# Kernel tuning notes

Measured on AMD Instinct MI355X. Metric: run time of the kernel, lower is better.

Reference implementation:

```python
import jax, jax.numpy as jnp
import numpy as np

N_NODES = 100000
N_EDGES = 1600000
D_IN = 128
D_HID = 128
D_OUT = 128
ORIG = 90000


def setup_inputs() -> dict:
    key = jax.random.key(0)
    ks = jax.random.split(key, 8)
    x = jax.random.normal(ks[0], (N_NODES, D_IN), dtype=jnp.float32)
    edge_index = jax.random.randint(ks[1], (2, N_EDGES), 0, N_NODES, dtype=jnp.int64)
    # Glorot-ish scaled weights; PyG SAGEConv: lin_l (with bias) on aggregated, lin_r (no bias) on root
    s1 = 1.0 / np.sqrt(D_IN)
    s2 = 1.0 / np.sqrt(D_HID)
    Wl1 = jax.random.normal(ks[2], (D_IN, D_HID), dtype=jnp.float32) * s1
    bl1 = jnp.zeros((D_HID,), dtype=jnp.float32)
    Wr1 = jax.random.normal(ks[3], (D_IN, D_HID), dtype=jnp.float32) * s1
    Wl2 = jax.random.normal(ks[4], (D_HID, D_OUT), dtype=jnp.float32) * s2
    bl2 = jnp.zeros((D_OUT,), dtype=jnp.float32)
    Wr2 = jax.random.normal(ks[5], (D_HID, D_OUT), dtype=jnp.float32) * s2
    return {"x": x, "edge_index": edge_index, "original_size": ORIG,
            "Wl1": Wl1, "bl1": bl1, "Wr1": Wr1,
            "Wl2": Wl2, "bl2": bl2, "Wr2": Wr2}


def _sage_conv(x, src, dst, Wl, bl, Wr):
    # PyG SAGEConv (aggr='mean'): out = lin_l(mean_{j in N(i)} x_j) + lin_r(x_i)
    n = x.shape[0]
    msgs = x[src]                                            # [E, d] gather
    ssum = jax.ops.segment_sum(msgs, dst, num_segments=n)    # [N, d]
    cnt = jax.ops.segment_sum(jnp.ones((src.shape[0],), dtype=x.dtype), dst,
                              num_segments=n)                # [N]
    mean = ssum / jnp.maximum(cnt, 1.0)[:, None]             # 0 for isolated nodes
    return mean @ Wl + bl + x @ Wr


def reference(x, edge_index, original_size, Wl1, bl1, Wr1, Wl2, bl2, Wr2):
    src, dst = edge_index[0], edge_index[1]
    h = _sage_conv(x, src, dst, Wl1, bl1, Wr1)
    h = _sage_conv(h, src, dst, Wl2, bl2, Wr2)
    return h[:original_size]
```

## Files before the change

### kernel.cpp

```cpp
#include <hip/hip_runtime.h>

#define NN 100000
#define DD 128

typedef __attribute__((ext_vector_type(8))) short bf16x8;
typedef __attribute__((ext_vector_type(4))) float f32x4;
typedef __attribute__((ext_vector_type(2))) float f32x2;

__device__ __forceinline__ float bf2f(unsigned short u) {
    union { unsigned int i; float f; } v;
    v.i = ((unsigned int)u) << 16;
    return v.f;
}

__device__ __forceinline__ unsigned short f2bf(float f) {
    union { float f; unsigned int i; } v;
    v.f = f;
    unsigned int x = v.i;
    return (unsigned short)((x + 0x7FFFu + ((x >> 16) & 1u)) >> 16);
}

__device__ __forceinline__ float2 load2(const float* p, int i2) {
    return ((const float2*)p)[i2];
}

__device__ __forceinline__ f32x2 cvt2(unsigned int u) {
    union { unsigned int i; float f; } lo, hi;
    lo.i = u << 16;
    hi.i = u & 0xffff0000u;
    return (f32x2){lo.f, hi.f};
}

__device__ __forceinline__ bf16x8 load8_bf(const unsigned short* p) {
    return *((const bf16x8*)p);
}
__device__ __forceinline__ bf16x8 load8_bf(const float* p) {
    float4 a = ((const float4*)p)[0];
    float4 b = ((const float4*)p)[1];
    bf16x8 r;
    r[0] = (short)f2bf(a.x); r[1] = (short)f2bf(a.y);
    r[2] = (short)f2bf(a.z); r[3] = (short)f2bf(a.w);
    r[4] = (short)f2bf(b.x); r[5] = (short)f2bf(b.y);
    r[6] = (short)f2bf(b.z); r[7] = (short)f2bf(b.w);
    return r;
}


#define PCH 16
#define NBUKMAX 512
#define CAP 12288

__global__ __launch_bounds__(256) void hist_buckets(
    const int* __restrict__ ei, int E, int* __restrict__ bcnt, int nbuk) {
    __shared__ int is64_s;
    __shared__ int hl[NBUKMAX];
    int tid = threadIdx.x;
    for (int i = tid; i < nbuk; i += 256) hl[i] = 0;
    if (tid < 64) {
        int ok = (ei[2 * tid + 1] == 0);
        int all = __all(ok);
        if (tid == 0) is64_s = all;
    }
    __syncthreads();
    int is64 = is64_s;
    int e0 = blockIdx.x * (256 * PCH) + tid;
#pragma unroll
    for (int c = 0; c < PCH; c++) {
        int e = e0 + c * 256;
        if (e < E) {
            int d = is64 ? ei[2 * (E + e)] : ei[E + e];
            atomicAdd(&hl[d >> 8], 1);
        }
    }
    __syncthreads();
    for (int i = tid; i < nbuk; i += 256) {
        int v = hl[i];
        if (v) atomicAdd(&bcnt[i], v);
    }
}

__global__ void scan_buckets(const int* __restrict__ bcnt, int nbuk,
                             int* __restrict__ boff, int* __restrict__ offN, int E) {
    __shared__ int wsum[8];
    int tid = threadIdx.x;
    int lane = tid & 63, wid = tid >> 6;
    int v = (tid < nbuk) ? bcnt[tid] : 0;
    int s = v;
#pragma unroll
    for (int dl = 1; dl < 64; dl <<= 1) {
        int t = __shfl_up(s, dl, 64);
        if (lane >= dl) s += t;
    }
    if (lane == 63) wsum[wid] = s;
    __syncthreads();
    int w = 0;
#pragma unroll
    for (int i = 0; i < 8; i++) w += (i < wid) ? wsum[i] : 0;
    if (tid < nbuk) boff[tid] = w + s - v;
    if (tid == nbuk - 1) boff[nbuk] = w + s;
    if (tid == 0) offN[0] = E;
}

__global__ __launch_bounds__(256) void partition_edges(
    const int* __restrict__ ei, int E, const int* __restrict__ boff,
    int* __restrict__ bcur, unsigned long long* __restrict__ pairs, int nbuk) {
    __shared__ int is64_s;
    __shared__ int cntb[NBUKMAX];
    __shared__ int baseb[NBUKMAX];
    __shared__ int boffb[NBUKMAX];
    int tid = threadIdx.x;
    for (int i = tid; i < nbuk; i += 256) {
        cntb[i] = 0;
        boffb[i] = boff[i];
    }
    if (tid < 64) {
        int ok = (ei[2 * tid + 1] == 0);
        int all = __all(ok);
        if (tid == 0) is64_s = all;
    }
    __syncthreads();
    int is64 = is64_s;
    int e0 = blockIdx.x * (256 * PCH) + tid;

    int dv[PCH], sv[PCH], bl[PCH];
    bool va[PCH];
#pragma unroll
    for (int c = 0; c < PCH; c++) {
        int e = e0 + c * 256;
        va[c] = (e < E);
        dv[c] = va[c] ? (is64 ? ei[2 * (E + e)] : ei[E + e]) : 0;
        sv[c] = va[c] ? (is64 ? ei[2 * e] : ei[e]) : 0;
        bl[c] = 0;
    }
#pragma unroll
    for (int c = 0; c < PCH; c++) {
        if (va[c]) {
            int b = dv[c] >> 8;
            int l = atomicAdd(&cntb[b], 1);
            bl[c] = (b << 16) | l;
        }
    }
    __syncthreads();
    for (int i = tid; i < nbuk; i += 256) {
        int cb = cntb[i];
        baseb[i] = cb ? atomicAdd(&bcur[i], cb) : 0;
    }
    __syncthreads();
#pragma unroll
    for (int c = 0; c < PCH; c++) {
        if (va[c]) {
            int b = bl[c] >> 16, l = bl[c] & 0xffff;
            pairs[(size_t)(boffb[b] + baseb[b] + l)] =
                ((unsigned long long)(unsigned int)dv[c] << 32) | (unsigned int)sv[c];
        }
    }
}

__global__ __launch_bounds__(256) void build_csr(
    const unsigned long long* __restrict__ pairs, const int* __restrict__ boff,
    int* __restrict__ off, int* __restrict__ csr, int* __restrict__ cur, int N) {
    int b = blockIdx.x;
    int lo = b << 8;
    if (lo >= N) return;
    int hi = min(lo + 256, N);
    int nn = hi - lo;
    int base = boff[b];
    int pcount = boff[b + 1] - base;

    __shared__ int cnt_l[256];
    __shared__ int start_l[256];
    __shared__ int cur_l[256];
    __shared__ int wsum[4];
    __shared__ int lds_csr[CAP];

    int tid = threadIdx.x;
    cnt_l[tid] = 0;
    __syncthreads();

    for (int i = tid; i < pcount; i += 256) {
        int d = (int)(pairs[base + i] >> 32);
        atomicAdd(&cnt_l[d - lo], 1);
    }
    __syncthreads();

    int v = cnt_l[tid];
    int s = v;
    int lane = tid & 63, wid = tid >> 6;
#pragma unroll
    for (int dl = 1; dl < 64; dl <<= 1) {
        int t = __shfl_up(s, dl, 64);
        if (lane >= dl) s += t;
    }
    if (lane == 63) wsum[wid] = s;
    __syncthreads();
    int w = 0;
#pragma unroll
    for (int i = 0; i < 4; i++) w += (i < wid) ? wsum[i] : 0;
    int excl = w + s - v;
    start_l[tid] = excl;
    cur_l[tid] = excl;
    if (tid < nn) off[lo + tid] = base + excl;
    __syncthreads();

    if (pcount <= CAP) {
        for (int i = tid; i < pcount; i += 256) {
            unsigned long long p = pairs[base + i];
            int d = (int)(p >> 32) - lo;
            int pos = atomicAdd(&cur_l[d], 1);
            lds_csr[pos] = (int)(p & 0xffffffffu);
        }
        __syncthreads();
        for (int i = tid; i < pcount; i += 256) csr[base + i] = lds_csr[i];
    } else {
        for (int i = tid; i < pcount; i += 256) {
            unsigned long long p = pairs[base + i];
            int dg = (int)(p >> 32);
            int q = atomicAdd(&cur[dg], 1);
            csr[base + start_l[dg - lo] + q] = (int)(p & 0xffffffffu);
        }
    }
}

__global__ void cast_bf16(const float* __restrict__ in, unsigned short* __restrict__ out,
                          int n4) {
    int i = blockIdx.x * blockDim.x + threadIdx.x;
    if (i >= n4) return;
    float4 v = ((const float4*)in)[i];
    ushort4 o;
    o.x = f2bf(v.x); o.y = f2bf(v.y); o.z = f2bf(v.z); o.w = f2bf(v.w);
    ((ushort4*)out)[i] = o;
}

__global__ void prep_weights(const float* __restrict__ Wl1, const float* __restrict__ Wr1,
                             const float* __restrict__ Wl2, const float* __restrict__ Wr2,
                             unsigned short* __restrict__ Wt1, unsigned short* __restrict__ Wt2) {
    __shared__ float t[32][33];
    int which = blockIdx.x >> 4;
    const float* W = (which == 0) ? Wl1 : (which == 1) ? Wr1 : (which == 2) ? Wl2 : Wr2;
    unsigned short* Wt = (which < 2) ? Wt1 : Wt2;
    int koff = (which & 1) * 128;
    int b = blockIdx.x & 15;
    int bx = b & 3, by = b >> 2;
    int c = threadIdx.x & 31, r8 = threadIdx.x >> 5;
#pragma unroll
    for (int i = 0; i < 4; i++) {
        int r = r8 + i * 8;
        t[r][c] = W[(by * 32 + r) * 128 + bx * 32 + c];
    }
    __syncthreads();
#pragma unroll
    for (int i = 0; i < 4; i++) {
        int r = r8 + i * 8;
        int fi = bx * 32 + r;
        int kk = koff + by * 32 + c;
        int idx = ((fi >> 4) * 8 + (kk >> 5)) * 512 + ((kk >> 3) & 3) * 128
                + (fi & 15) * 8 + (kk & 7);
        Wt[idx] = f2bf(t[c][r]);
    }
}

#define ACC8(u) do { \
    acc[0] += cvt2((u).x); acc[1] += cvt2((u).y); \
    acc[2] += cvt2((u).z); acc[3] += cvt2((u).w); } while (0)

__global__ __launch_bounds__(256) void aggregate_bf(
    const unsigned short* __restrict__ feat,
    const int* __restrict__ off, const int* __restrict__ csr,
    unsigned short* __restrict__ mean, int N, const int* __restrict__ limp) {
    int lim = limp ? min(N, limp[0]) : N;
    int node = blockIdx.x * 4 + (threadIdx.x >> 6);
    if (node >= lim) return;
    int lane = threadIdx.x & 63;
    int e = lane >> 4, q = lane & 15;
    int s0 = off[node], s1 = off[node + 1];
    unsigned qoff = (unsigned)q << 4;
    const char* fb = (const char*)feat;

    f32x2 acc[4];
#pragma unroll
    for (int t = 0; t < 4; t++) acc[t] = (f32x2){0.f, 0.f};

    for (int c0 = s0; c0 < s1; c0 += 64) {
        int cdeg = min(64, s1 - c0);
        int cr = (lane < cdeg) ? csr[c0 + lane] : 0;
        int nfull = cdeg >> 4, rem = cdeg & 15;
        for (int b = 0; b < nfull; b++) {
            int i0 = b * 16 + e;
            unsigned o0 = ((unsigned)__shfl(cr, i0, 64) << 8) + qoff;
            unsigned o1 = ((unsigned)__shfl(cr, i0 + 4, 64) << 8) + qoff;
            unsigned o2 = ((unsigned)__shfl(cr, i0 + 8, 64) << 8) + qoff;
            unsigned o3 = ((unsigned)__shfl(cr, i0 + 12, 64) << 8) + qoff;
            uint4 C0 = *(const uint4*)(fb + o0);
            uint4 C1 = *(const uint4*)(fb + o1);
            uint4 C2 = *(const uint4*)(fb + o2);
            uint4 C3 = *(const uint4*)(fb + o3);
            ACC8(C0); ACC8(C1); ACC8(C2); ACC8(C3);
        }
        if (rem) {
            int i0 = nfull * 16 + e;
            int t0 = __shfl(cr, i0, 64), t1 = __shfl(cr, i0 + 4, 64),
                t2 = __shfl(cr, i0 + 8, 64), t3 = __shfl(cr, i0 + 12, 64);
            uint4 C0 = make_uint4(0, 0, 0, 0), C1 = C0, C2 = C0, C3 = C0;
            if (i0 < cdeg)      C0 = *(const uint4*)(fb + ((((unsigned)t0) << 8) + qoff));
            if (i0 + 4 < cdeg)  C1 = *(const uint4*)(fb + ((((unsigned)t1) << 8) + qoff));
            if (i0 + 8 < cdeg)  C2 = *(const uint4*)(fb + ((((unsigned)t2) << 8) + qoff));
            if (i0 + 12 < cdeg) C3 = *(const uint4*)(fb + ((((unsigned)t3) << 8) + qoff));
            ACC8(C0); ACC8(C1); ACC8(C2); ACC8(C3);
        }
    }

#pragma unroll
    for (int t = 0; t < 4; t++) {
        union { f32x2 v; double d; } a, b;
        a.v = acc[t];
        b.d = __shfl_xor(a.d, 16, 64); a.v += b.v;
        b.d = __shfl_xor(a.d, 32, 64); a.v += b.v;
        acc[t] = a.v;
    }

    int deg = s1 - s0;
    float inv = (deg > 0) ? (1.0f / (float)deg) : 0.0f;
    if (e == 0) {
        f32x2 iv = (f32x2){inv, inv};
        f32x2 m0 = acc[0] * iv, m1 = acc[1] * iv,
              m2 = acc[2] * iv, m3 = acc[3] * iv;
        uint4 w;
        asm("v_cvt_pk_bf16_f32 %0, %1, %2" : "=v"(w.x) : "v"(m0.x), "v"(m0.y));
        asm("v_cvt_pk_bf16_f32 %0, %1, %2" : "=v"(w.y) : "v"(m1.x), "v"(m1.y));
        asm("v_cvt_pk_bf16_f32 %0, %1, %2" : "=v"(w.z) : "v"(m2.x), "v"(m2.y));
        asm("v_cvt_pk_bf16_f32 %0, %1, %2" : "=v"(w.w) : "v"(m3.x), "v"(m3.y));
        *((uint4*)((char*)mean + (size_t)node * 256 + qoff)) = w;
    }
}

__global__ void aggregate_f32(const float* __restrict__ feat,
                              const int* __restrict__ off, const int* __restrict__ csr,
                              unsigned short* __restrict__ mean, int N) {
    int node = blockIdx.x * (blockDim.x >> 6) + (threadIdx.x >> 6);
    if (node >= N) return;
    int lane = threadIdx.x & 63;
    int s0 = off[node], s1 = off[node + 1];
    float ax = 0.f, ay = 0.f;
    for (int j = s0; j < s1; j++) {
        int s = csr[j];
        float2 v = load2(feat, s * 64 + lane);
        ax += v.x; ay += v.y;
    }
    float inv = (s1 > s0) ? (1.0f / (float)(s1 - s0)) : 0.0f;
    unsigned int p = (unsigned int)f2bf(ax * inv) | ((unsigned int)f2bf(ay * inv) << 16);
    ((unsigned int*)mean)[node * 64 + lane] = p;
}

template <typename TA2, typename TO>
__global__ __launch_bounds__(256) void gemm_mfma(
    const unsigned short* __restrict__ A1, const TA2* __restrict__ A2,
    const unsigned short* __restrict__ Wt, const float* __restrict__ bias,
    TO* __restrict__ out, int Arows, int Nlimit, const int* __restrict__ origp) {
    int lim = Nlimit;
    if (origp) lim = min(lim, origp[0]);
    int n0 = blockIdx.x * 64;
    if (n0 >= lim) return;

    int tid = threadIdx.x;
    int lane = tid & 63;
    int wid = tid >> 6;
    int wm = wid >> 1, wn = wid & 1;
    int qd = lane >> 4, l16 = lane & 15;

    int r0 = min(n0 + wm * 32 + l16, Arows - 1);
    int r1 = min(n0 + wm * 32 + 16 + l16, Arows - 1);

    f32x4 acc[2][4];
#pragma unroll
    for (int a = 0; a < 2; a++)
#pragma unroll
        for (int b = 0; b < 4; b++) acc[a][b] = (f32x4){0.f, 0.f, 0.f, 0.f};

#pragma unroll
    for (int ks = 0; ks < 8; ks++) {
        int kb = (ks & 3) * 32;
        bf16x8 a0, a1;
        if (ks < 4) {
            a0 = load8_bf(A1 + (size_t)r0 * 128 + kb + qd * 8);
            a1 = load8_bf(A1 + (size_t)r1 * 128 + kb + qd * 8);
        } else {
            a0 = load8_bf(A2 + (size_t)r0 * 128 + kb + qd * 8);
            a1 = load8_bf(A2 + (size_t)r1 * 128 + kb + qd * 8);
        }
#pragma unroll
        for (int tn = 0; tn < 4; tn++) {
            int slot = (wn * 4 + tn) * 8 + ks;
            bf16x8 bfrag = *((const bf16x8*)(Wt + slot * 512 + lane * 8));
            acc[0][tn] = __builtin_amdgcn_mfma_f32_16x16x32_bf16(a0, bfrag, acc[0][tn], 0, 0, 0);
            acc[1][tn] = __builtin_amdgcn_mfma_f32_16x16x32_bf16(a1, bfrag, acc[1][tn], 0, 0, 0);
        }
    }

#pragma unroll
    for (int tn = 0; tn < 4; tn++) {
        int f = wn * 64 + tn * 16 + l16;
        float bv = bias[f];
#pragma unroll
        for (int tm = 0; tm < 2; tm++) {
#pragma unroll
            for (int r = 0; r < 4; r++) {
                int n = n0 + wm * 32 + tm * 16 + qd * 4 + r;
                if (n < lim) {
                    float val = acc[tm][tn][r] + bv;
                    if constexpr (__is_same(TO, float))
                        out[n * 128 + f] = val;
                    else
                        out[n * 128 + f] = f2bf(val);
                }
            }
        }
    }
}

extern "C" void kernel_launch(void* const* d_in, const int* in_sizes, int n_in,
                              void* d_out, int out_size, void* d_ws, size_t ws_size,
                              hipStream_t stream) {
    const float* x   = (const float*)d_in[0];
    const int*   ei  = (const int*)d_in[1];
    const int*   org = (const int*)d_in[2];
    const float* Wl1 = (const float*)d_in[3];
    const float* bl1 = (const float*)d_in[4];
    const float* Wr1 = (const float*)d_in[5];
    const float* Wl2 = (const float*)d_in[6];
    const float* bl2 = (const float*)d_in[7];
    const float* Wr2 = (const float*)d_in[8];
    float* out = (float*)d_out;

    const int N = in_sizes[0] / DD;
    const int E = in_sizes[1] / 2;

    size_t szFeat = (size_t)N * DD * 2;
    size_t szBase = 2 * szFeat
                  + 2 * 65536
                  + (size_t)N * 4 + 4096
                  + (size_t)(N + 1) * 4
                  + 4096
                  + (size_t)E * 4;
    bool big = ws_size >= szBase + szFeat + 4096;

    char* ws = (char*)d_ws;
    unsigned short* mean = (unsigned short*)ws;  ws += szFeat;
    unsigned short* h    = (unsigned short*)ws;  ws += szFeat;
    unsigned short* xb   = nullptr;
    if (big) { xb = (unsigned short*)ws; ws += szFeat; }
    unsigned short* Wt1 = (unsigned short*)ws;  ws += 65536;
    unsigned short* Wt2 = (unsigned short*)ws;  ws += 65536;
    int* cur  = (int*)ws;  ws += (size_t)N * 4;
    int* bcnt = (int*)ws;  ws += 2048;
    int* bcur = (int*)ws;  ws += 2048;
    int* off  = (int*)ws;  ws += (size_t)(N + 1) * 4;
    int* boff = (int*)ws;  ws += 4096;
    int* csr  = (int*)ws;

    unsigned long long* pairs = (unsigned long long*)mean;

    int nbuk = (N + 255) >> 8;
    int edgeGrid = (E + 256 * PCH - 1) / (256 * PCH);

    hipMemsetAsync(cur, 0, (size_t)N * 4 + 4096, stream);
    hist_buckets<<<edgeGrid, 256, 0, stream>>>(ei, E, bcnt, nbuk);
    scan_buckets<<<1, 512, 0, stream>>>(bcnt, nbuk, boff, off + N, E);
    partition_edges<<<edgeGrid, 256, 0, stream>>>(ei, E, boff, bcur, pairs, nbuk);
    build_csr<<<nbuk, 256, 0, stream>>>(pairs, boff, off, csr, cur, N);

    prep_weights<<<64, 256, 0, stream>>>(Wl1, Wr1, Wl2, Wr2, Wt1, Wt2);

    int aggGrid  = (N + 3) / 4;
    int gemmGrid = (N + 63) / 64;

    if (big) {
        cast_bf16<<<(N * DD / 4 + 255) / 256, 256, 0, stream>>>(x, xb, N * DD / 4);
        aggregate_bf<<<aggGrid, 256, 0, stream>>>(xb, off, csr, mean, N, nullptr);
        gemm_mfma<unsigned short, unsigned short><<<gemmGrid, 256, 0, stream>>>(
            mean, xb, Wt1, bl1, h, N, N, nullptr);
    } else {
        aggregate_f32<<<aggGrid, 256, 0, stream>>>(x, off, csr, mean, N);
        gemm_mfma<float, unsigned short><<<gemmGrid, 256, 0, stream>>>(
            mean, x, Wt1, bl1, h, N, N, nullptr);
    }
    aggregate_bf<<<aggGrid, 256, 0, stream>>>(h, off, csr, mean, N, org);
    gemm_mfma<unsigned short, float><<<gemmGrid, 256, 0, stream>>>(
        mean, h, Wt2, bl2, out, N, N, org);
}
```

Measured before the change: 331.9 us.

## Split bf16 aggregation across 8 feature-slice blocks per node group

```diff
diff --git a/kernel.cpp b/kernel.cpp
--- a/kernel.cpp
+++ b/kernel.cpp
@@ -259,21 +259,18 @@
     }
 }
 
-#define ACC8(u) do { \
-    acc[0] += cvt2((u).x); acc[1] += cvt2((u).y); \
-    acc[2] += cvt2((u).z); acc[3] += cvt2((u).w); } while (0)
-
 __global__ __launch_bounds__(256) void aggregate_bf(
     const unsigned short* __restrict__ feat,
     const int* __restrict__ off, const int* __restrict__ csr,
     unsigned short* __restrict__ mean, int N, const int* __restrict__ limp) {
     int lim = limp ? min(N, limp[0]) : N;
-    int node = blockIdx.x * 4 + (threadIdx.x >> 6);
+    int slice = blockIdx.x & 7;
+    int node = (blockIdx.x >> 3) * 4 + (threadIdx.x >> 6);
     if (node >= lim) return;
     int lane = threadIdx.x & 63;
-    int e = lane >> 4, q = lane & 15;
+    int e = lane >> 1, q = lane & 1;
     int s0 = off[node], s1 = off[node + 1];
-    unsigned qoff = (unsigned)q << 4;
+    unsigned qoff = (unsigned)(slice * 32 + q * 16);
     const char* fb = (const char*)feat;
 
     f32x2 acc[4];
@@ -282,30 +279,23 @@
 
     for (int c0 = s0; c0 < s1; c0 += 64) {
         int cdeg = min(64, s1 - c0);
-        int cr = (lane < cdeg) ? csr[c0 + lane] : 0;
-        int nfull = cdeg >> 4, rem = cdeg & 15;
+        int cr = 0;
+        if (lane < cdeg) cr = __builtin_nontemporal_load(&csr[c0 + lane]);
+        int nfull = cdeg >> 5, rem = cdeg & 31;
         for (int b = 0; b < nfull; b++) {
-            int i0 = b * 16 + e;
+            int i0 = b * 32 + e;
             unsigned o0 = ((unsigned)__shfl(cr, i0, 64) << 8) + qoff;
-            unsigned o1 = ((unsigned)__shfl(cr, i0 + 4, 64) << 8) + qoff;
-            unsigned o2 = ((unsigned)__shfl(cr, i0 + 8, 64) << 8) + qoff;
-            unsigned o3 = ((unsigned)__shfl(cr, i0 + 12, 64) << 8) + qoff;
             uint4 C0 = *(const uint4*)(fb + o0);
-            uint4 C1 = *(const uint4*)(fb + o1);
-            uint4 C2 = *(const uint4*)(fb + o2);
-            uint4 C3 = *(const uint4*)(fb + o3);
-            ACC8(C0); ACC8(C1); ACC8(C2); ACC8(C3);
+            acc[0] += cvt2(C0.x); acc[1] += cvt2(C0.y);
+            acc[2] += cvt2(C0.z); acc[3] += cvt2(C0.w);
         }
         if (rem) {
-            int i0 = nfull * 16 + e;
-            int t0 = __shfl(cr, i0, 64), t1 = __shfl(cr, i0 + 4, 64),
-                t2 = __shfl(cr, i0 + 8, 64), t3 = __shfl(cr, i0 + 12, 64);
-            uint4 C0 = make_uint4(0, 0, 0, 0), C1 = C0, C2 = C0, C3 = C0;
-            if (i0 < cdeg)      C0 = *(const uint4*)(fb + ((((unsigned)t0) << 8) + qoff));
-            if (i0 + 4 < cdeg)  C1 = *(const uint4*)(fb + ((((unsigned)t1) << 8) + qoff));
-            if (i0 + 8 < cdeg)  C2 = *(const uint4*)(fb + ((((unsigned)t2) << 8) + qoff));
-            if (i0 + 12 < cdeg) C3 = *(const uint4*)(fb + ((((unsigned)t3) << 8) + qoff));
-            ACC8(C0); ACC8(C1); ACC8(C2); ACC8(C3);
+            int i0 = nfull * 32 + e;
+            int t0 = __shfl(cr, i0, 64);
+            uint4 C0 = make_uint4(0, 0, 0, 0);
+            if (i0 < cdeg) C0 = *(const uint4*)(fb + ((((unsigned)t0) << 8) + qoff));
+            acc[0] += cvt2(C0.x); acc[1] += cvt2(C0.y);
+            acc[2] += cvt2(C0.z); acc[3] += cvt2(C0.w);
         }
     }
 
@@ -313,6 +303,9 @@
     for (int t = 0; t < 4; t++) {
         union { f32x2 v; double d; } a, b;
         a.v = acc[t];
+        b.d = __shfl_xor(a.d, 2, 64);  a.v += b.v;
+        b.d = __shfl_xor(a.d, 4, 64);  a.v += b.v;
+        b.d = __shfl_xor(a.d, 8, 64);  a.v += b.v;
         b.d = __shfl_xor(a.d, 16, 64); a.v += b.v;
         b.d = __shfl_xor(a.d, 32, 64); a.v += b.v;
         acc[t] = a.v;
@@ -470,7 +463,8 @@
 
     prep_weights<<<64, 256, 0, stream>>>(Wl1, Wr1, Wl2, Wr2, Wt1, Wt2);
 
-    int aggGrid  = (N + 3) / 4;
+    int aggGrid  = ((N + 3) / 4) * 8;
+    int aggGridF = (N + 3) / 4;
     int gemmGrid = (N + 63) / 64;
 
     if (big) {
@@ -479,7 +473,7 @@
         gemm_mfma<unsigned short, unsigned short><<<gemmGrid, 256, 0, stream>>>(
             mean, xb, Wt1, bl1, h, N, N, nullptr);
     } else {
-        aggregate_f32<<<aggGrid, 256, 0, stream>>>(x, off, csr, mean, N);
+        aggregate_f32<<<aggGridF, 256, 0, stream>>>(x, off, csr, mean, N);
         gemm_mfma<float, unsigned short><<<gemmGrid, 256, 0, stream>>>(
             mean, x, Wt1, bl1, h, N, N, nullptr);
     }
```

Result: slower. 866.1 us (+161.0%).
